# Optimization experiments

Measured on AMD Instinct MI355X. Metric: run time of the kernel, lower is better.

Reference implementation:

```python
import jax, jax.numpy as jnp
import numpy as np

EARLY_ROUND = 6
LATE_ROUND = 12
NUM_CLASSES = 35


def setup_inputs() -> dict:
    key = jax.random.key(0)
    k1, k2, k3 = jax.random.split(key, 3)
    B = 1048576
    logits = jax.random.normal(k1, (B, NUM_CLASSES), dtype=jnp.float32)
    targets = jax.random.randint(k2, (B,), 0, NUM_CLASSES, dtype=jnp.int64)
    turns = jax.random.randint(k3, (B,), 0, 24, dtype=jnp.int64)
    return {"logits": logits, "targets": targets, "turns": turns}


def reference(logits, targets, turns):
    # per-sample cross entropy (reduction='none')
    logp = jax.nn.log_softmax(logits, axis=-1)  # [B, C]
    losses = -jnp.take_along_axis(logp, targets[:, None], axis=-1)[:, 0]  # [B]
    # piecewise-linear weight: 0.7 for turn<=early, 1.0 for turn>=late, lerp between
    t = turns.astype(logits.dtype)
    frac = (t - EARLY_ROUND) / (LATE_ROUND - EARLY_ROUND)
    weights = jnp.clip(0.7 + 0.3 * frac, 0.7, 1.0)
    return jnp.mean(losses * weights)
```

## Files before the change

kernel.cpp:

```cpp
#include <hip/hip_runtime.h>
#include <math.h>

#define NUM_CLASSES 35
#define CHUNKS 4
#define NBLOCKS 1024

__global__ __launch_bounds__(256) void fuzzy_loss_pass1(
    const float* __restrict__ logits,
    const int* __restrict__ targets,
    const int* __restrict__ turns,
    float* __restrict__ partial)
{
    __shared__ float lds[4 * 64 * NUM_CLASSES];
    const int tid  = threadIdx.x;
    const int wave = tid >> 6;
    const int lane = tid & 63;
    float* wlds = lds + wave * (64 * NUM_CLASSES);
    const int blk_row0 = blockIdx.x * (256 * CHUNKS);

    float4 r[9];

    auto load_chunk = [&](int c) {
        const float4* g = (const float4*)logits
                        + ((size_t)(blk_row0 + c * 256 + wave * 64) * NUM_CLASSES) / 4;
        #pragma unroll
        for (int i = 0; i < 8; ++i) r[i] = g[i * 64 + lane];
        if (lane < 48) r[8] = g[512 + lane];
    };
    auto store_chunk = [&]() {
        float4* d = (float4*)wlds;
        #pragma unroll
        for (int i = 0; i < 8; ++i) d[i * 64 + lane] = r[i];
        if (lane < 48) d[512 + lane] = r[8];
    };

    float v = 0.0f;
    load_chunk(0);
    store_chunk();

    #pragma unroll
    for (int c = 0; c < CHUNKS; ++c) {
        const int row = blk_row0 + c * 256 + wave * 64 + lane;
        const int   tgt = targets[row];
        const float t   = (float)turns[row];

        if (c + 1 < CHUNKS) load_chunk(c + 1);

        const float* myrow = wlds + lane * NUM_CLASSES;
        float s0 = 0.f, s1 = 0.f, s2 = 0.f, s3 = 0.f;
        #pragma unroll
        for (int j = 0; j < 32; j += 4) {
            s0 += __expf(myrow[j]);     s1 += __expf(myrow[j + 1]);
            s2 += __expf(myrow[j + 2]); s3 += __expf(myrow[j + 3]);
        }
        s0 += __expf(myrow[32]); s1 += __expf(myrow[33]); s2 += __expf(myrow[34]);
        const float xt = myrow[tgt];
        float loss = __logf((s0 + s1) + (s2 + s3)) - xt;

        float w = fmaf(0.05f, t, 0.4f);
        w = fminf(fmaxf(w, 0.7f), 1.0f);
        v = fmaf(loss, w, v);

        if (c + 1 < CHUNKS) store_chunk();
    }

    #pragma unroll
    for (int off = 32; off > 0; off >>= 1)
        v += __shfl_down(v, off, 64);
    if (lane == 0) partial[blockIdx.x * 4 + wave] = v;
}

__global__ __launch_bounds__(256) void fuzzy_loss_pass2(
    const float* __restrict__ partial,
    float* __restrict__ out,
    int n, float inv_B)
{
    const int tid = threadIdx.x;
    float v = 0.0f;
    const float4* src = (const float4*)partial;
    for (int i = tid; i < n / 4; i += 256) {
        float4 f = src[i];
        v += (f.x + f.y) + (f.z + f.w);
    }
    #pragma unroll
    for (int off = 32; off > 0; off >>= 1)
        v += __shfl_down(v, off, 64);

    __shared__ float wsum[4];
    if ((tid & 63) == 0) wsum[tid >> 6] = v;
    __syncthreads();
    if (tid == 0)
        out[0] = (wsum[0] + wsum[1] + wsum[2] + wsum[3]) * inv_B;
}

extern "C" void kernel_launch(void* const* d_in, const int* in_sizes, int n_in,
                              void* d_out, int out_size, void* d_ws, size_t ws_size,
                              hipStream_t stream) {
    const float* logits  = (const float*)d_in[0];
    const int*   targets = (const int*)d_in[1];
    const int*   turns   = (const int*)d_in[2];
    float*       out     = (float*)d_out;
    float*       partial = (float*)d_ws;

    const int B = in_sizes[1];

    fuzzy_loss_pass1<<<NBLOCKS, 256, 0, stream>>>(logits, targets, turns, partial);
    fuzzy_loss_pass2<<<1, 256, 0, stream>>>(partial, out, NBLOCKS * 4, 1.0f / (float)B);
}
```

Baseline: 241.0 us.

## Compute row exp-sums directly from coalesced float4 loads with LDS atomics

Replaces the staging of full logit tiles in LDS with exponentiation directly on coalesced float4 loads. Each lane splits its four exps across the row boundary and accumulates per-row sums into a small shared array with LDS atomics. The target logit is then gathered from global memory. This cuts LDS footprint, which should raise occupancy, and removes the LDS store/reload of every logit. In exchange it adds many shared atomics, drops the explicit next-chunk prefetch, and adds a scattered global gather. Reads of rs between tiles have no explicit wave barrier, relying on wave-synchronous execution.

```diff
diff --git a/kernel.cpp b/kernel.cpp
--- a/kernel.cpp
+++ b/kernel.cpp
@@ -2,72 +2,74 @@
 #include <math.h>
 
 #define NUM_CLASSES 35
-#define CHUNKS 4
+#define BLOCK 256
 #define NBLOCKS 1024
+#define TILES_PER_WAVE 4
 
-__global__ __launch_bounds__(256) void fuzzy_loss_pass1(
+__global__ __launch_bounds__(BLOCK, 4) void fuzzy_loss_pass1(
     const float* __restrict__ logits,
     const int* __restrict__ targets,
     const int* __restrict__ turns,
     float* __restrict__ partial)
 {
-    __shared__ float lds[4 * 64 * NUM_CLASSES];
+    __shared__ float rowsum[4][64];
     const int tid  = threadIdx.x;
     const int wave = tid >> 6;
     const int lane = tid & 63;
-    float* wlds = lds + wave * (64 * NUM_CLASSES);
-    const int blk_row0 = blockIdx.x * (256 * CHUNKS);
+    float* rs = rowsum[wave];
 
-    float4 r[9];
+    const int gwave = blockIdx.x * 4 + wave;
+    float v = 0.0f;
 
-    auto load_chunk = [&](int c) {
-        const float4* g = (const float4*)logits
-                        + ((size_t)(blk_row0 + c * 256 + wave * 64) * NUM_CLASSES) / 4;
-        #pragma unroll
-        for (int i = 0; i < 8; ++i) r[i] = g[i * 64 + lane];
-        if (lane < 48) r[8] = g[512 + lane];
-    };
-    auto store_chunk = [&]() {
-        float4* d = (float4*)wlds;
-        #pragma unroll
-        for (int i = 0; i < 8; ++i) d[i * 64 + lane] = r[i];
-        if (lane < 48) d[512 + lane] = r[8];
-    };
+    #pragma unroll 2
+    for (int tIdx = 0; tIdx < TILES_PER_WAVE; ++tIdx) {
+        const int tile = gwave * TILES_PER_WAVE + tIdx;
+        const int r0   = tile * 64;
+        const size_t f0 = (size_t)tile * 560;
 
-    float v = 0.0f;
-    load_chunk(0);
-    store_chunk();
+        rs[lane] = 0.0f;
 
-    #pragma unroll
-    for (int c = 0; c < CHUNKS; ++c) {
-        const int row = blk_row0 + c * 256 + wave * 64 + lane;
+        const int row = r0 + lane;
         const int   tgt = targets[row];
         const float t   = (float)turns[row];
+        const int   ft  = row * NUM_CLASSES + tgt;
 
-        if (c + 1 < CHUNKS) load_chunk(c + 1);
+        int rloc = (4 * lane) / 35;
+        int p    = (4 * lane) - rloc * 35;
 
-        const float* myrow = wlds + lane * NUM_CLASSES;
-        float s0 = 0.f, s1 = 0.f, s2 = 0.f, s3 = 0.f;
+        const float4* src = (const float4*)logits + f0;
         #pragma unroll
-        for (int j = 0; j < 32; j += 4) {
-            s0 += __expf(myrow[j]);     s1 += __expf(myrow[j + 1]);
-            s2 += __expf(myrow[j + 2]); s3 += __expf(myrow[j + 3]);
+        for (int i = 0; i < 9; ++i) {
+            if (i < 8 || lane < 48) {
+                float4 q = src[i * 64 + lane];
+                float e0 = __expf(q.x), e1 = __expf(q.y);
+                float e2 = __expf(q.z), e3 = __expf(q.w);
+                int b = 35 - p;
+                float slo = e0;
+                slo += (b > 1) ? e1 : 0.0f;
+                slo += (b > 2) ? e2 : 0.0f;
+                slo += (b > 3) ? e3 : 0.0f;
+                float shi = ((e0 + e1) + (e2 + e3)) - slo;
+                atomicAdd(&rs[rloc], slo);
+                if (b < 4) atomicAdd(&rs[rloc + 1], shi);
+                p += 11; rloc += 7;
+                if (p >= 35) { p -= 35; rloc += 1; }
+            }
         }
-        s0 += __expf(myrow[32]); s1 += __expf(myrow[33]); s2 += __expf(myrow[34]);
-        const float xt = myrow[tgt];
-        float loss = __logf((s0 + s1) + (s2 + s3)) - xt;
 
+        float s = rs[lane];
+        const float xt = logits[ft];
+        float loss = __logf(s) - xt;
         float w = fmaf(0.05f, t, 0.4f);
         w = fminf(fmaxf(w, 0.7f), 1.0f);
         v = fmaf(loss, w, v);
-
-        if (c + 1 < CHUNKS) store_chunk();
     }
 
     #pragma unroll
     for (int off = 32; off > 0; off >>= 1)
         v += __shfl_down(v, off, 64);
-    if (lane == 0) partial[blockIdx.x * 4 + wave] = v;
+    if (lane == 0)
+        partial[gwave] = v;
 }
 
 __global__ __launch_bounds__(256) void fuzzy_loss_pass2(
@@ -104,6 +106,6 @@
 
     const int B = in_sizes[1];
 
-    fuzzy_loss_pass1<<<NBLOCKS, 256, 0, stream>>>(logits, targets, turns, partial);
+    fuzzy_loss_pass1<<<NBLOCKS, BLOCK, 0, stream>>>(logits, targets, turns, partial);
     fuzzy_loss_pass2<<<1, 256, 0, stream>>>(partial, out, NBLOCKS * 4, 1.0f / (float)B);
 }
```

New measurement: 228.1 us. 1.06x faster.
